# Performance work log

Measured on AMD Instinct MI355X. Metric: run time of the kernel, lower is better.

## Reference

```python
import jax, jax.numpy as jnp
import numpy as np

MARGIN = 0.3
LAMBDA_TRIPLET = 1.0
LAMBDA_ID = 1.0
EPS = 1e-6  # torch pairwise_distance eps added to the difference elementwise


def setup_inputs() -> dict:
    key = jax.random.key(0)
    k1, k2 = jax.random.split(key)
    B, N, D = 64, 512, 512
    reid_features = jax.random.normal(k1, (B, N, D), dtype=jnp.float32)
    # ids in [-1, 32): -1 marks invalid detections, as in the torch module
    track_ids = jax.random.randint(k2, (B, N), -1, 32, dtype=jnp.int32)
    return {"reid_features": reid_features, "track_ids": track_ids}


def _tracking_loss(feats, ids, margin):
    B, N, D = feats.shape
    valid = ids >= 0                                   # (B, N)
    same = ids[:, :, None] == ids[:, None, :]          # (B, N, N)
    not_self = ~jnp.eye(N, dtype=bool)                 # (N, N)
    valid_j = valid[:, None, :]                        # candidates must be valid
    pos_mask = same & not_self & valid_j               # (B, N, N)
    neg_mask = (~same) & valid_j                       # (B, N, N)
    has_pos = pos_mask.any(-1)                         # (B, N)
    has_neg = neg_mask.any(-1)
    enough = valid.sum(-1) >= 2                        # (B,)
    anchor_ok = valid & has_pos & has_neg & enough[:, None]
    # torch.nonzero(mask)[0] == first True index -> argmax on bool
    pos_idx = jnp.argmax(pos_mask, axis=-1)            # (B, N)
    neg_idx = jnp.argmax(neg_mask, axis=-1)
    p = jnp.take_along_axis(feats, pos_idx[..., None], axis=1)  # (B, N, D)
    n = jnp.take_along_axis(feats, neg_idx[..., None], axis=1)
    d_ap = jnp.sqrt(jnp.sum((feats - p + EPS) ** 2, axis=-1))   # (B, N)
    d_an = jnp.sqrt(jnp.sum((feats - n + EPS) ** 2, axis=-1))
    per_anchor = jnp.maximum(d_ap - d_an + margin, 0.0)
    num_triplets = anchor_ok.sum()
    total = jnp.sum(per_anchor * anchor_ok.astype(feats.dtype))
    loss = jnp.where(num_triplets > 0,
                     total / jnp.maximum(num_triplets, 1).astype(feats.dtype),
                     jnp.zeros((), feats.dtype))
    return loss * LAMBDA_TRIPLET


def reference(reid_features, track_ids):
    loss_triplet = _tracking_loss(reid_features, track_ids, MARGIN)
    loss_id = jnp.zeros((), reid_features.dtype)
    tracking_loss = loss_triplet + loss_id
    return tracking_loss, loss_triplet, loss_id
```

## Files before the change

### kernel.cpp

```cpp
#include <hip/hip_runtime.h>

#define MARGIN 0.3f
#define EPS 1e-6f

constexpr int B = 64, N = 512, D = 512;
constexpr int NIDS = 32;

constexpr int MB_THREADS = 512;
constexpr int MB_WAVES = MB_THREADS / 64;
constexpr int ANCH_PER_WAVE = 8;
constexpr int A_BLOCK = MB_WAVES * ANCH_PER_WAVE;
constexpr int MB_BLOCKS = (B * N) / A_BLOCK;


__global__ __launch_bounds__(MB_THREADS) void tl_main(const float* __restrict__ feats,
                                                      const int* __restrict__ ids,
                                                      float* __restrict__ psum,
                                                      float* __restrict__ pcnt) {
    __shared__ int s_ids[N];
    __shared__ int s_first[NIDS], s_second[NIDS];
    __shared__ int s_j0, s_jdiff, s_vcnt;
    __shared__ float s_wsum[MB_WAVES];
    __shared__ int s_wcnt[MB_WAVES];

    const int t = threadIdx.x;
    const int lane = t & 63;
    const int wave = t >> 6;

    const int logical = ((blockIdx.x & 7) << 6) | (blockIdx.x >> 3);
    const int b = logical >> 3;
    const int seg = (logical & 7) * A_BLOCK;
    const float* __restrict__ bf = feats + (size_t)b * N * D;

    if (t < NIDS) { s_first[t] = N; s_second[t] = N; }
    if (t == 0) { s_j0 = N; s_jdiff = N; s_vcnt = 0; }
    __syncthreads();

    const int v = ids[b * N + t];
    s_ids[t] = v;
    const unsigned long long m = __ballot(v >= 0);
    if (lane == 0) atomicAdd(&s_vcnt, __popcll(m));
    if (v >= 0) {
        atomicMin(&s_first[v], t);
        atomicMin(&s_j0, t);
    }
    __syncthreads();
    const int id0 = (s_j0 < N) ? s_ids[s_j0] : -2;
    if (v >= 0) {
        if (s_first[v] != t) atomicMin(&s_second[v], t);
        if (v != id0) atomicMin(&s_jdiff, t);
    }
    __syncthreads();

    const int vcnt = s_vcnt;
    const int j0 = min(s_j0, N - 1), jdiff = min(s_jdiff, N - 1);

    const float4* n0p = (const float4*)(bf + (size_t)j0 * D) + lane * 2;
    const float4* n1p = (const float4*)(bf + (size_t)jdiff * D) + lane * 2;
    const float4 n0a = n0p[0], n0b = n0p[1];
    const float4 n1a = n1p[0], n1b = n1p[1];

    float wsum = 0.0f;
    int wcnt = 0;

    #pragma unroll
    for (int c = 0; c < ANCH_PER_WAVE / 4; ++c) {
        const int base = seg + wave * ANCH_PER_WAVE + c * 4;

        int pj[4]; bool okk[4]; bool useN0[4];
        #pragma unroll
        for (int k = 0; k < 4; ++k) {
            const int i = base + k;
            const int vi = s_ids[i];
            bool ok = (vi >= 0) && (vcnt >= 2);
            int posj = 0, negj = 0;
            if (ok) {
                posj = (s_first[vi] != i) ? s_first[vi] : s_second[vi];
                negj = (vi != id0) ? s_j0 : s_jdiff;
                ok = (posj < N) && (negj < N);
            }
            okk[k] = ok;
            pj[k] = ok ? posj : 0;
            useN0[k] = (negj == s_j0);
        }

        float4 A0[4], A1[4], P0[4], P1[4];
        #pragma unroll
        for (int k = 0; k < 4; ++k) {
            const int i = base + k;
            const float4* fa = (const float4*)(bf + (size_t)i * D) + lane * 2;
            const float4* fp = (const float4*)(bf + (size_t)pj[k] * D) + lane * 2;
            A0[k] = fa[0]; A1[k] = fa[1];
            P0[k] = fp[0]; P1[k] = fp[1];
        }

        #pragma unroll
        for (int k = 0; k < 4; ++k) {
            const float4 m0 = useN0[k] ? n0a : n1a;
            const float4 m1 = useN0[k] ? n0b : n1b;
            float sap = 0.0f, san = 0.0f, dd;
            dd = A0[k].x - P0[k].x + EPS; sap += dd * dd;
            dd = A0[k].y - P0[k].y + EPS; sap += dd * dd;
            dd = A0[k].z - P0[k].z + EPS; sap += dd * dd;
            dd = A0[k].w - P0[k].w + EPS; sap += dd * dd;
            dd = A1[k].x - P1[k].x + EPS; sap += dd * dd;
            dd = A1[k].y - P1[k].y + EPS; sap += dd * dd;
            dd = A1[k].z - P1[k].z + EPS; sap += dd * dd;
            dd = A1[k].w - P1[k].w + EPS; sap += dd * dd;
            dd = A0[k].x - m0.x + EPS; san += dd * dd;
            dd = A0[k].y - m0.y + EPS; san += dd * dd;
            dd = A0[k].z - m0.z + EPS; san += dd * dd;
            dd = A0[k].w - m0.w + EPS; san += dd * dd;
            dd = A1[k].x - m1.x + EPS; san += dd * dd;
            dd = A1[k].y - m1.y + EPS; san += dd * dd;
            dd = A1[k].z - m1.z + EPS; san += dd * dd;
            dd = A1[k].w - m1.w + EPS; san += dd * dd;

            #pragma unroll
            for (int off = 32; off >= 1; off >>= 1) {
                sap += __shfl_xor(sap, off);
                san += __shfl_xor(san, off);
            }
            const float per = fmaxf(sqrtf(sap) - sqrtf(san) + MARGIN, 0.0f);
            wsum += okk[k] ? per : 0.0f;
            wcnt += okk[k] ? 1 : 0;
        }
    }

    if (lane == 0) { s_wsum[wave] = wsum; s_wcnt[wave] = wcnt; }
    __syncthreads();
    if (t == 0) {
        float s = 0.0f; int c = 0;
        #pragma unroll
        for (int w = 0; w < MB_WAVES; ++w) { s += s_wsum[w]; c += s_wcnt[w]; }
        psum[blockIdx.x] = s;
        pcnt[blockIdx.x] = (float)c;
    }
}

__global__ __launch_bounds__(256) void tl_finalize(const float* __restrict__ psum,
                                                   const float* __restrict__ pcnt,
                                                   float* __restrict__ out) {
    __shared__ float s_s[4], s_c[4];
    const int t = threadIdx.x;
    float s = 0.0f, c = 0.0f;
    for (int k = t; k < MB_BLOCKS; k += 256) { s += psum[k]; c += pcnt[k]; }
    #pragma unroll
    for (int off = 32; off >= 1; off >>= 1) {
        s += __shfl_xor(s, off);
        c += __shfl_xor(c, off);
    }
    if ((t & 63) == 0) { s_s[t >> 6] = s; s_c[t >> 6] = c; }
    __syncthreads();
    if (t == 0) {
        const float S = s_s[0] + s_s[1] + s_s[2] + s_s[3];
        const float C = s_c[0] + s_c[1] + s_c[2] + s_c[3];
        const float loss = (C > 0.0f) ? (S / C) : 0.0f;
        out[0] = loss;
        out[1] = loss;
        out[2] = 0.0f;
    }
}

extern "C" void kernel_launch(void* const* d_in, const int* in_sizes, int n_in,
                              void* d_out, int out_size, void* d_ws, size_t ws_size,
                              hipStream_t stream) {
    const float* feats = (const float*)d_in[0];
    const int* ids = (const int*)d_in[1];
    float* out = (float*)d_out;

    float* psum = (float*)d_ws;
    float* pcnt = psum + MB_BLOCKS;

    tl_main<<<MB_BLOCKS, MB_THREADS, 0, stream>>>(feats, ids, psum, pcnt);
    tl_finalize<<<1, 256, 0, stream>>>(psum, pcnt, out);
}
```

Measured before the change: 103.3 us.

## Prefetch anchor rows before id scan and shrink blocks to 256 threads

Anchor feature loads are issued at kernel start, before the shared-memory id histogram and first/second-index search, so their global-memory latency overlaps the barriers and atomics. Blocks shrink to 256 threads with 4 anchors per wave, giving 4x more blocks, and each thread now scans two ids. The per-block id scan is repeated across more blocks, which adds redundant ids reads and atomics.

```diff
diff --git a/kernel.cpp b/kernel.cpp
--- a/kernel.cpp
+++ b/kernel.cpp
@@ -6,9 +6,9 @@
 constexpr int B = 64, N = 512, D = 512;
 constexpr int NIDS = 32;
 
-constexpr int MB_THREADS = 512;
+constexpr int MB_THREADS = 256;
 constexpr int MB_WAVES = MB_THREADS / 64;
-constexpr int ANCH_PER_WAVE = 8;
+constexpr int ANCH_PER_WAVE = 4;
 constexpr int A_BLOCK = MB_WAVES * ANCH_PER_WAVE;
 constexpr int MB_BLOCKS = (B * N) / A_BLOCK;
 
@@ -27,104 +27,108 @@
     const int lane = t & 63;
     const int wave = t >> 6;
 
-    const int logical = ((blockIdx.x & 7) << 6) | (blockIdx.x >> 3);
-    const int b = logical >> 3;
-    const int seg = (logical & 7) * A_BLOCK;
+    const int logical = ((blockIdx.x & 7) << 8) | (blockIdx.x >> 3);
+    const int b = logical >> 5;
+    const int seg = (logical & 31) * A_BLOCK;
     const float* __restrict__ bf = feats + (size_t)b * N * D;
+
+    float4 A0[ANCH_PER_WAVE], A1[ANCH_PER_WAVE];
+    #pragma unroll
+    for (int k = 0; k < ANCH_PER_WAVE; ++k) {
+        const int i = seg + wave * ANCH_PER_WAVE + k;
+        const float4* fa = (const float4*)(bf + (size_t)i * D) + lane * 2;
+        A0[k] = fa[0]; A1[k] = fa[1];
+    }
 
     if (t < NIDS) { s_first[t] = N; s_second[t] = N; }
     if (t == 0) { s_j0 = N; s_jdiff = N; s_vcnt = 0; }
     __syncthreads();
 
-    const int v = ids[b * N + t];
-    s_ids[t] = v;
-    const unsigned long long m = __ballot(v >= 0);
-    if (lane == 0) atomicAdd(&s_vcnt, __popcll(m));
-    if (v >= 0) {
-        atomicMin(&s_first[v], t);
-        atomicMin(&s_j0, t);
-    }
+    const int v1 = ids[b * N + t];
+    const int v2 = ids[b * N + t + 256];
+    s_ids[t] = v1;
+    s_ids[t + 256] = v2;
+    const unsigned long long m1 = __ballot(v1 >= 0);
+    const unsigned long long m2 = __ballot(v2 >= 0);
+    if (lane == 0) atomicAdd(&s_vcnt, __popcll(m1) + __popcll(m2));
+    if (v1 >= 0) { atomicMin(&s_first[v1], t);       atomicMin(&s_j0, t); }
+    if (v2 >= 0) { atomicMin(&s_first[v2], t + 256); atomicMin(&s_j0, t + 256); }
     __syncthreads();
     const int id0 = (s_j0 < N) ? s_ids[s_j0] : -2;
-    if (v >= 0) {
-        if (s_first[v] != t) atomicMin(&s_second[v], t);
-        if (v != id0) atomicMin(&s_jdiff, t);
+    if (v1 >= 0) {
+        if (s_first[v1] != t) atomicMin(&s_second[v1], t);
+        if (v1 != id0) atomicMin(&s_jdiff, t);
+    }
+    if (v2 >= 0) {
+        if (s_first[v2] != t + 256) atomicMin(&s_second[v2], t + 256);
+        if (v2 != id0) atomicMin(&s_jdiff, t + 256);
     }
     __syncthreads();
 
     const int vcnt = s_vcnt;
-    const int j0 = min(s_j0, N - 1), jdiff = min(s_jdiff, N - 1);
+    const int j0c = min(s_j0, N - 1), jdc = min(s_jdiff, N - 1);
 
-    const float4* n0p = (const float4*)(bf + (size_t)j0 * D) + lane * 2;
-    const float4* n1p = (const float4*)(bf + (size_t)jdiff * D) + lane * 2;
+    const float4* n0p = (const float4*)(bf + (size_t)j0c * D) + lane * 2;
+    const float4* n1p = (const float4*)(bf + (size_t)jdc * D) + lane * 2;
     const float4 n0a = n0p[0], n0b = n0p[1];
     const float4 n1a = n1p[0], n1b = n1p[1];
 
+    int pj[ANCH_PER_WAVE]; bool okk[ANCH_PER_WAVE]; bool useN0[ANCH_PER_WAVE];
+    #pragma unroll
+    for (int k = 0; k < ANCH_PER_WAVE; ++k) {
+        const int i = seg + wave * ANCH_PER_WAVE + k;
+        const int vi = s_ids[i];
+        bool ok = (vi >= 0) && (vcnt >= 2);
+        int posj = 0, negj = -1;
+        if (ok) {
+            posj = (s_first[vi] != i) ? s_first[vi] : s_second[vi];
+            negj = (vi != id0) ? s_j0 : s_jdiff;
+            ok = (posj < N) && (negj < N);
+        }
+        okk[k] = ok;
+        pj[k] = ok ? posj : 0;
+        useN0[k] = (negj == s_j0);
+    }
+
+    float4 P0[ANCH_PER_WAVE], P1[ANCH_PER_WAVE];
+    #pragma unroll
+    for (int k = 0; k < ANCH_PER_WAVE; ++k) {
+        const float4* fp = (const float4*)(bf + (size_t)pj[k] * D) + lane * 2;
+        P0[k] = fp[0]; P1[k] = fp[1];
+    }
+
     float wsum = 0.0f;
     int wcnt = 0;
-
     #pragma unroll
-    for (int c = 0; c < ANCH_PER_WAVE / 4; ++c) {
-        const int base = seg + wave * ANCH_PER_WAVE + c * 4;
-
-        int pj[4]; bool okk[4]; bool useN0[4];
-        #pragma unroll
-        for (int k = 0; k < 4; ++k) {
-            const int i = base + k;
-            const int vi = s_ids[i];
-            bool ok = (vi >= 0) && (vcnt >= 2);
-            int posj = 0, negj = 0;
-            if (ok) {
-                posj = (s_first[vi] != i) ? s_first[vi] : s_second[vi];
-                negj = (vi != id0) ? s_j0 : s_jdiff;
-                ok = (posj < N) && (negj < N);
-            }
-            okk[k] = ok;
-            pj[k] = ok ? posj : 0;
-            useN0[k] = (negj == s_j0);
-        }
-
-        float4 A0[4], A1[4], P0[4], P1[4];
-        #pragma unroll
-        for (int k = 0; k < 4; ++k) {
-            const int i = base + k;
-            const float4* fa = (const float4*)(bf + (size_t)i * D) + lane * 2;
-            const float4* fp = (const float4*)(bf + (size_t)pj[k] * D) + lane * 2;
-            A0[k] = fa[0]; A1[k] = fa[1];
-            P0[k] = fp[0]; P1[k] = fp[1];
-        }
+    for (int k = 0; k < ANCH_PER_WAVE; ++k) {
+        const float4 m0 = useN0[k] ? n0a : n1a;
+        const float4 m1v = useN0[k] ? n0b : n1b;
+        float sap = 0.0f, san = 0.0f, dd;
+        dd = A0[k].x - P0[k].x + EPS; sap += dd * dd;
+        dd = A0[k].y - P0[k].y + EPS; sap += dd * dd;
+        dd = A0[k].z - P0[k].z + EPS; sap += dd * dd;
+        dd = A0[k].w - P0[k].w + EPS; sap += dd * dd;
+        dd = A1[k].x - P1[k].x + EPS; sap += dd * dd;
+        dd = A1[k].y - P1[k].y + EPS; sap += dd * dd;
+        dd = A1[k].z - P1[k].z + EPS; sap += dd * dd;
+        dd = A1[k].w - P1[k].w + EPS; sap += dd * dd;
+        dd = A0[k].x - m0.x + EPS; san += dd * dd;
+        dd = A0[k].y - m0.y + EPS; san += dd * dd;
+        dd = A0[k].z - m0.z + EPS; san += dd * dd;
+        dd = A0[k].w - m0.w + EPS; san += dd * dd;
+        dd = A1[k].x - m1v.x + EPS; san += dd * dd;
+        dd = A1[k].y - m1v.y + EPS; san += dd * dd;
+        dd = A1[k].z - m1v.z + EPS; san += dd * dd;
+        dd = A1[k].w - m1v.w + EPS; san += dd * dd;
 
         #pragma unroll
-        for (int k = 0; k < 4; ++k) {
-            const float4 m0 = useN0[k] ? n0a : n1a;
-            const float4 m1 = useN0[k] ? n0b : n1b;
-            float sap = 0.0f, san = 0.0f, dd;
-            dd = A0[k].x - P0[k].x + EPS; sap += dd * dd;
-            dd = A0[k].y - P0[k].y + EPS; sap += dd * dd;
-            dd = A0[k].z - P0[k].z + EPS; sap += dd * dd;
-            dd = A0[k].w - P0[k].w + EPS; sap += dd * dd;
-            dd = A1[k].x - P1[k].x + EPS; sap += dd * dd;
-            dd = A1[k].y - P1[k].y + EPS; sap += dd * dd;
-            dd = A1[k].z - P1[k].z + EPS; sap += dd * dd;
-            dd = A1[k].w - P1[k].w + EPS; sap += dd * dd;
-            dd = A0[k].x - m0.x + EPS; san += dd * dd;
-            dd = A0[k].y - m0.y + EPS; san += dd * dd;
-            dd = A0[k].z - m0.z + EPS; san += dd * dd;
-            dd = A0[k].w - m0.w + EPS; san += dd * dd;
-            dd = A1[k].x - m1.x + EPS; san += dd * dd;
-            dd = A1[k].y - m1.y + EPS; san += dd * dd;
-            dd = A1[k].z - m1.z + EPS; san += dd * dd;
-            dd = A1[k].w - m1.w + EPS; san += dd * dd;
-
-            #pragma unroll
-            for (int off = 32; off >= 1; off >>= 1) {
-                sap += __shfl_xor(sap, off);
-                san += __shfl_xor(san, off);
-            }
-            const float per = fmaxf(sqrtf(sap) - sqrtf(san) + MARGIN, 0.0f);
-            wsum += okk[k] ? per : 0.0f;
-            wcnt += okk[k] ? 1 : 0;
+        for (int off = 32; off >= 1; off >>= 1) {
+            sap += __shfl_xor(sap, off);
+            san += __shfl_xor(san, off);
         }
+        const float per = fmaxf(sqrtf(sap) - sqrtf(san) + MARGIN, 0.0f);
+        wsum += okk[k] ? per : 0.0f;
+        wcnt += okk[k] ? 1 : 0;
     }
 
     if (lane == 0) { s_wsum[wave] = wsum; s_wcnt[wave] = wcnt; }
```

After: 115.7 us. 1.12x slower.

## Precompute per-batch positive/negative index tables in a separate kernel

Applied to the files above, without the earlier changes.

Moves the per-batch id scan (first/second occurrence per id, first valid, first differing index, valid count) out of every main block into a small kernel run once per batch that writes compact tables to workspace. The main kernel then loads only the 68-entry table and its own anchors' ids. Blocks shrink from 512 to 256 threads with twice as many blocks, and the block swizzle is updated to match. This removes the redundant 512-id scan and its atomics and barriers from all 512 main blocks, at the cost of one extra kernel launch and a global round trip for the tables.

```diff
diff --git a/kernel.cpp b/kernel.cpp
--- a/kernel.cpp
+++ b/kernel.cpp
@@ -5,32 +5,22 @@
 
 constexpr int B = 64, N = 512, D = 512;
 constexpr int NIDS = 32;
-
-constexpr int MB_THREADS = 512;
+constexpr int TAB = 68;
+
+constexpr int MB_THREADS = 256;
 constexpr int MB_WAVES = MB_THREADS / 64;
 constexpr int ANCH_PER_WAVE = 8;
 constexpr int A_BLOCK = MB_WAVES * ANCH_PER_WAVE;
 constexpr int MB_BLOCKS = (B * N) / A_BLOCK;
 
 
-__global__ __launch_bounds__(MB_THREADS) void tl_main(const float* __restrict__ feats,
-                                                      const int* __restrict__ ids,
-                                                      float* __restrict__ psum,
-                                                      float* __restrict__ pcnt) {
+__global__ __launch_bounds__(512) void tl_tables(const int* __restrict__ ids,
+                                                 int* __restrict__ tabs) {
     __shared__ int s_ids[N];
     __shared__ int s_first[NIDS], s_second[NIDS];
     __shared__ int s_j0, s_jdiff, s_vcnt;
-    __shared__ float s_wsum[MB_WAVES];
-    __shared__ int s_wcnt[MB_WAVES];
-
     const int t = threadIdx.x;
-    const int lane = t & 63;
-    const int wave = t >> 6;
-
-    const int logical = ((blockIdx.x & 7) << 6) | (blockIdx.x >> 3);
-    const int b = logical >> 3;
-    const int seg = (logical & 7) * A_BLOCK;
-    const float* __restrict__ bf = feats + (size_t)b * N * D;
+    const int b = blockIdx.x;
 
     if (t < NIDS) { s_first[t] = N; s_second[t] = N; }
     if (t == 0) { s_j0 = N; s_jdiff = N; s_vcnt = 0; }
@@ -39,7 +29,7 @@
     const int v = ids[b * N + t];
     s_ids[t] = v;
     const unsigned long long m = __ballot(v >= 0);
-    if (lane == 0) atomicAdd(&s_vcnt, __popcll(m));
+    if ((t & 63) == 0) atomicAdd(&s_vcnt, __popcll(m));
     if (v >= 0) {
         atomicMin(&s_first[v], t);
         atomicMin(&s_j0, t);
@@ -52,11 +42,43 @@
     }
     __syncthreads();
 
-    const int vcnt = s_vcnt;
-    const int j0 = min(s_j0, N - 1), jdiff = min(s_jdiff, N - 1);
-
-    const float4* n0p = (const float4*)(bf + (size_t)j0 * D) + lane * 2;
-    const float4* n1p = (const float4*)(bf + (size_t)jdiff * D) + lane * 2;
+    int* tb = tabs + b * TAB;
+    if (t < NIDS)            tb[t] = s_first[t];
+    else if (t < 2 * NIDS)   tb[t] = s_second[t - NIDS];
+    else if (t == 64)        tb[64] = s_j0;
+    else if (t == 65)        tb[65] = s_jdiff;
+    else if (t == 66)        tb[66] = s_vcnt;
+    else if (t == 67)        tb[67] = id0;
+}
+
+__global__ __launch_bounds__(MB_THREADS) void tl_main(const float* __restrict__ feats,
+                                                      const int* __restrict__ ids,
+                                                      const int* __restrict__ tabs,
+                                                      float* __restrict__ psum,
+                                                      float* __restrict__ pcnt) {
+    __shared__ int s_tab[TAB];
+    __shared__ int s_aids[A_BLOCK];
+    __shared__ float s_wsum[MB_WAVES];
+    __shared__ int s_wcnt[MB_WAVES];
+
+    const int t = threadIdx.x;
+    const int lane = t & 63;
+    const int wave = t >> 6;
+
+    const int logical = ((blockIdx.x & 7) << 7) | (blockIdx.x >> 3);
+    const int b = logical >> 4;
+    const int seg = (logical & 15) * A_BLOCK;
+    const float* __restrict__ bf = feats + (size_t)b * N * D;
+
+    if (t < TAB) s_tab[t] = tabs[b * TAB + t];
+    if (t < A_BLOCK) s_aids[t] = ids[b * N + seg + t];
+    __syncthreads();
+
+    const int j0 = s_tab[64], jdiff = s_tab[65], vcnt = s_tab[66], id0 = s_tab[67];
+    const int j0c = min(j0, N - 1), jdc = min(jdiff, N - 1);
+
+    const float4* n0p = (const float4*)(bf + (size_t)j0c * D) + lane * 2;
+    const float4* n1p = (const float4*)(bf + (size_t)jdc * D) + lane * 2;
     const float4 n0a = n0p[0], n0b = n0p[1];
     const float4 n1a = n1p[0], n1b = n1p[1];
 
@@ -65,29 +87,31 @@
 
     #pragma unroll
     for (int c = 0; c < ANCH_PER_WAVE / 4; ++c) {
-        const int base = seg + wave * ANCH_PER_WAVE + c * 4;
+        const int lbase = wave * ANCH_PER_WAVE + c * 4;
 
         int pj[4]; bool okk[4]; bool useN0[4];
         #pragma unroll
         for (int k = 0; k < 4; ++k) {
-            const int i = base + k;
-            const int vi = s_ids[i];
+            const int li = lbase + k;
+            const int i = seg + li;
+            const int vi = s_aids[li];
             bool ok = (vi >= 0) && (vcnt >= 2);
             int posj = 0, negj = 0;
             if (ok) {
-                posj = (s_first[vi] != i) ? s_first[vi] : s_second[vi];
-                negj = (vi != id0) ? s_j0 : s_jdiff;
+                const int f = s_tab[vi];
+                posj = (f != i) ? f : s_tab[NIDS + vi];
+                negj = (vi != id0) ? j0 : jdiff;
                 ok = (posj < N) && (negj < N);
             }
             okk[k] = ok;
             pj[k] = ok ? posj : 0;
-            useN0[k] = (negj == s_j0);
+            useN0[k] = (negj == j0);
         }
 
         float4 A0[4], A1[4], P0[4], P1[4];
         #pragma unroll
         for (int k = 0; k < 4; ++k) {
-            const int i = base + k;
+            const int i = seg + lbase + k;
             const float4* fa = (const float4*)(bf + (size_t)i * D) + lane * 2;
             const float4* fp = (const float4*)(bf + (size_t)pj[k] * D) + lane * 2;
             A0[k] = fa[0]; A1[k] = fa[1];
@@ -169,9 +193,12 @@
     const int* ids = (const int*)d_in[1];
     float* out = (float*)d_out;
 
-    float* psum = (float*)d_ws;
+    char* ws = (char*)d_ws;
+    int* tabs = (int*)ws;
+    float* psum = (float*)(ws + sizeof(int) * B * TAB);
     float* pcnt = psum + MB_BLOCKS;
 
-    tl_main<<<MB_BLOCKS, MB_THREADS, 0, stream>>>(feats, ids, psum, pcnt);
+    tl_tables<<<B, 512, 0, stream>>>(ids, tabs);
+    tl_main<<<MB_BLOCKS, MB_THREADS, 0, stream>>>(feats, ids, tabs, psum, pcnt);
     tl_finalize<<<1, 256, 0, stream>>>(psum, pcnt, out);
 }
```

New measurement: 102.6 us, median of 2. No clear change (-0.6%).
